# Kernel optimization log

Hardware: AMD Instinct MI355X
Metric: run time of the kernel (lower is better)

The kernel has to match this reference:

```python
import jax, jax.numpy as jnp
import numpy as np

L, D, F, H = 6, 512, 2048, 8
DH = D // H
SCALE = DH ** -0.5
B, S = 2, 2048


def _ln(x, w, b):
    m = jnp.mean(x, axis=-1, keepdims=True)
    v = jnp.var(x, axis=-1, keepdims=True)
    return (x - m) * jax.lax.rsqrt(v + 1e-5) * w + b


def setup_inputs() -> dict:
    key = jax.random.key(0)
    ks = jax.random.split(key, 10)
    s = 0.02
    return {
        "x": jax.random.normal(ks[0], (B, S, D), jnp.float32),
        "mask": jnp.zeros((B, 1, 1, S), jnp.float32),
        "ln1_w": jnp.ones((L, D), jnp.float32),
        "ln1_b": jnp.zeros((L, D), jnp.float32),
        "in_w": s * jax.random.normal(ks[1], (L, D, 3 * D), jnp.float32),
        "in_b": jnp.zeros((L, 3 * D), jnp.float32),
        "out_w": s * jax.random.normal(ks[2], (L, D, D), jnp.float32),
        "out_b": jnp.zeros((L, D), jnp.float32),
        "ln2_w": jnp.ones((L, D), jnp.float32),
        "ln2_b": jnp.zeros((L, D), jnp.float32),
        "ffn1_w": s * jax.random.normal(ks[3], (L, D, F), jnp.float32),
        "ffn1_b": jnp.zeros((L, F), jnp.float32),
        "ffn2_w": s * jax.random.normal(ks[4], (L, F, D), jnp.float32),
        "ffn2_b": jnp.zeros((L, D), jnp.float32),
        "norm_w": jnp.ones((D,), jnp.float32),
        "norm_b": jnp.zeros((D,), jnp.float32),
    }


def reference(x, mask, ln1_w, ln1_b, in_w, in_b, out_w, out_b,
              ln2_w, ln2_b, ffn1_w, ffn1_b, ffn2_w, ffn2_b, norm_w, norm_b):
    def step(h, p):
        (l1w, l1b, iw, ib, ow, ob, l2w, l2b, f1w, f1b, f2w, f2b) = p
        # --- self-attention (pre-norm) ---
        y = _ln(h, l1w, l1b)
        proj = y @ iw + ib                       # [B,S,3D]
        q, k, v = jnp.split(proj, 3, axis=-1)    # each [B,S,D]
        q = q.reshape(B, S, H, DH)
        k = k.reshape(B, S, H, DH)
        v = v.reshape(B, S, H, DH)
        dot = jnp.einsum('bqhd,bkhd->bhqk', q * SCALE, k) + mask  # [B,H,S,S]
        att = jax.nn.softmax(dot, axis=-1)
        o = jnp.einsum('bhqk,bkhd->bqhd', att, v).reshape(B, S, D)
        h = o @ ow + ob + h
        # --- FFN (pre-norm) ---
        y = _ln(h, l2w, l2b)
        y = jax.nn.relu(y @ f1w + f1b) @ f2w + f2b
        return h + y, None

    params = (ln1_w, ln1_b, in_w, in_b, out_w, out_b,
              ln2_w, ln2_b, ffn1_w, ffn1_b, ffn2_w, ffn2_b)
    x, _ = jax.lax.scan(step, x, params)
    return _ln(x, norm_w, norm_b)
```

## Files before the change

kernel.cpp:

```cpp
#include <hip/hip_runtime.h>
#include <hip/hip_bf16.h>
#include <stdint.h>


typedef __bf16 bf16x8 __attribute__((ext_vector_type(8)));
typedef __bf16 bf16x4 __attribute__((ext_vector_type(4)));
typedef float f32x4 __attribute__((ext_vector_type(4)));
typedef unsigned short u16;
typedef unsigned short u16x8 __attribute__((ext_vector_type(8)));

#define NB 2
#define NS 2048
#define ND 512
#define NH 8
#define NDH 64
#define NF 2048
#define NL 6
#define NCHUNK 4
#define CK (NS / NCHUNK)
#define LOG2E 1.4426950408889634f
#define QSCALE (0.125f * LOG2E)

#if defined(__has_builtin)
#if __has_builtin(__builtin_amdgcn_global_load_lds)
#define HAVE_GLDS 1
#endif
#endif
#ifndef HAVE_GLDS
#define HAVE_GLDS 0
#endif

#if HAVE_GLDS
__device__ __forceinline__ void glds16(const u16* g, u16* l) {
  __builtin_amdgcn_global_load_lds(
      (const __attribute__((address_space(1))) unsigned int*)g,
      (__attribute__((address_space(3))) unsigned int*)l, 16, 0, 0);
}
#endif

__device__ __forceinline__ u16 f2bf(float f) {
  unsigned u = __float_as_uint(f);
  u += 0x7FFFu + ((u >> 16) & 1u);
  return (u16)(u >> 16);
}

__device__ __forceinline__ int xswz(int w, int n) {
  return (w & 7) * (n >> 3) + (w >> 3);
}

__global__ __launch_bounds__(256) void wcvt_t(const float* __restrict__ src,
                                              u16* __restrict__ dst,
                                              int K, int N) {
  __shared__ float tile[32][33];
  int l = blockIdx.z;
  const float* s = src + (size_t)l * K * N;
  u16* d = dst + (size_t)l * K * N;
  int k0 = blockIdx.y * 32, n0 = blockIdx.x * 32;
  int tx = threadIdx.x, ty = threadIdx.y;
  for (int i = 0; i < 32; i += 8)
    tile[ty + i][tx] = s[(size_t)(k0 + ty + i) * N + n0 + tx];
  __syncthreads();
  for (int i = 0; i < 32; i += 8)
    d[(size_t)(n0 + ty + i) * K + k0 + tx] = f2bf(tile[tx][ty + i]);
}

template <int OUT_BF16>
__global__ __launch_bounds__(256) void ln_k(const float* __restrict__ x,
                                            const float* __restrict__ w,
                                            const float* __restrict__ b,
                                            void* __restrict__ out) {
  int row = blockIdx.x;
  int t = threadIdx.x;
  const float* xr = x + (size_t)row * ND;
  float2 v = ((const float2*)xr)[t];
  float s = v.x + v.y, ss = v.x * v.x + v.y * v.y;
  for (int o = 32; o > 0; o >>= 1) {
    s += __shfl_down(s, o);
    ss += __shfl_down(ss, o);
  }
  __shared__ float rs[4], rss[4];
  if ((t & 63) == 0) { rs[t >> 6] = s; rss[t >> 6] = ss; }
  __syncthreads();
  float S = rs[0] + rs[1] + rs[2] + rs[3];
  float SS = rss[0] + rss[1] + rss[2] + rss[3];
  float mean = S * (1.0f / ND);
  float var = SS * (1.0f / ND) - mean * mean;
  float rstd = rsqrtf(var + 1e-5f);
  float2 wv = ((const float2*)w)[t];
  float2 bv = ((const float2*)b)[t];
  float y0 = (v.x - mean) * rstd * wv.x + bv.x;
  float y1 = (v.y - mean) * rstd * wv.y + bv.y;
  if (OUT_BF16) {
    ushort2 p; p.x = f2bf(y0); p.y = f2bf(y1);
    ((ushort2*)out)[(size_t)row * (ND / 2) + t] = p;
  } else {
    float2 p; p.x = y0; p.y = y1;
    ((float2*)out)[(size_t)row * (ND / 2) + t] = p;
  }
}

template <int EPI, int BM, int BN, int BK>
__global__ __launch_bounds__(256) void gemm_bt(const u16* __restrict__ A,
                                               const u16* __restrict__ Bt,
                                               const float* __restrict__ bias,
                                               const float* __restrict__ resid,
                                               void* __restrict__ C,
                                               int M, int N, int K) {
  constexpr int MT = BM / 32;
  constexpr int NT = BN / 32;
  constexpr int CB = BK / 8;
  constexpr int RPP = 2048 / BK;
  constexpr int AP = BM / RPP;
  constexpr int BP = BN / RPP;
  constexpr int KK = BK / 32;
  __shared__ u16 la[2][BM * BK];
  __shared__ u16 lb[2][BN * BK];
  int flat = blockIdx.x + gridDim.x * blockIdx.y;
  int s_id = xswz(flat, gridDim.x * gridDim.y);
  int bn = s_id % gridDim.x, bm = s_id / gridDim.x;
  int t = threadIdx.x;
  int wave = t >> 6, lane = t & 63, quad = lane >> 4, l15 = lane & 15;
  int wm = (wave >> 1) * (BM / 2), wn = (wave & 1) * (BN / 2);
  f32x4 acc[MT][NT] = {};
  int srow = t / CB;
  int scol = ((t % CB) ^ (srow & (CB - 1))) * 8;
  const u16* Ag = A + (size_t)(bm * BM) * K;
  const u16* Bg = Bt + (size_t)(bn * BN) * K;

  auto stage = [&](int k0, int buf) {
#if HAVE_GLDS
    u16* laB = &la[buf][0] + wave * 512;
    u16* lbB = &lb[buf][0] + wave * 512;
#pragma unroll
    for (int g = 0; g < AP; g++)
      glds16(&Ag[(size_t)(srow + g * RPP) * K + k0 + scol], laB + g * 2048);
#pragma unroll
    for (int g = 0; g < BP; g++)
      glds16(&Bg[(size_t)(srow + g * RPP) * K + k0 + scol], lbB + g * 2048);
#else
#pragma unroll
    for (int g = 0; g < AP; g++)
      *(bf16x8*)&la[buf][(srow + g * RPP) * BK + (t % CB) * 8] =
          *(const bf16x8*)&Ag[(size_t)(srow + g * RPP) * K + k0 + scol];
#pragma unroll
    for (int g = 0; g < BP; g++)
      *(bf16x8*)&lb[buf][(srow + g * RPP) * BK + (t % CB) * 8] =
          *(const bf16x8*)&Bg[(size_t)(srow + g * RPP) * K + k0 + scol];
#endif
  };

  stage(0, 0);
  const int nk = K / BK;
  int cur = 0;
  for (int ks = 0; ks < nk; ks++) {
    __syncthreads();
    if (ks + 1 < nk) stage((ks + 1) * BK, cur ^ 1);
    const u16* lac = &la[cur][0];
    const u16* lbc = &lb[cur][0];
#pragma unroll
    for (int kk = 0; kk < KK; kk++) {
      bf16x8 af[MT], bfr[NT];
#pragma unroll
      for (int i = 0; i < MT; i++) {
        int row = wm + i * 16 + l15;
        af[i] = *(const bf16x8*)&lac[row * BK + ((kk * 4 + quad) ^ (row & (CB - 1))) * 8];
      }
#pragma unroll
      for (int i = 0; i < NT; i++) {
        int row = wn + i * 16 + l15;
        bfr[i] = *(const bf16x8*)&lbc[row * BK + ((kk * 4 + quad) ^ (row & (CB - 1))) * 8];
      }
#pragma unroll
      for (int mt = 0; mt < MT; mt++)
#pragma unroll
        for (int nt = 0; nt < NT; nt++)
          acc[mt][nt] = __builtin_amdgcn_mfma_f32_16x16x32_bf16(
              af[mt], bfr[nt], acc[mt][nt], 0, 0, 0);
    }
    cur ^= 1;
  }
#pragma unroll
  for (int mt = 0; mt < MT; mt++)
#pragma unroll
    for (int nt = 0; nt < NT; nt++) {
      int col = bn * BN + wn + nt * 16 + l15;
      float bcol = (EPI == 3) ? 0.f : bias[col];
#pragma unroll
      for (int r = 0; r < 4; r++) {
        int row = bm * BM + wm + mt * 16 + quad * 4 + r;
        float v = acc[mt][nt][r] + ((EPI == 3) ? bias[row] : bcol);
        if (EPI == 1) v = fmaxf(v, 0.f);
        if (EPI == 2)
          ((float*)C)[(size_t)row * N + col] = v + resid[(size_t)row * N + col];
        else
          ((u16*)C)[(size_t)row * N + col] = f2bf(v);
      }
    }
}

__global__ __launch_bounds__(256) void attn_k(const u16* __restrict__ qk,
                                              const u16* __restrict__ vt,
                                              const float* __restrict__ mask,
                                              u16* __restrict__ opart,
                                              float* __restrict__ lbuf) {
  __shared__ u16 kt_s[64 * 64];
  __shared__ u16 vt_s[64 * 64];
  __shared__ u16 p_s[4][16 * 64];
  __shared__ float mask_s[CK];
  int flat = blockIdx.x + 32 * (blockIdx.y + 16 * blockIdx.z);
  int s_id = xswz(flat, 32 * 16 * NCHUNK);
  int qt = s_id & 31;
  int bh = (s_id >> 5) & 15;
  int c = s_id >> 9;
  int b = bh >> 3, h = bh & 7;
  int t = threadIdx.x;
  int wave = t >> 6, lane = t & 63, quad = lane >> 4, l15 = lane & 15;

  {
    const float* mrow = mask + b * NS + c * CK;
    mask_s[t] = mrow[t] * LOG2E;
    mask_s[t + 256] = mrow[t + 256] * LOG2E;
  }

  int qrow = qt * 64 + wave * 16 + l15;
  const u16* qbase = qk + ((size_t)(b * NS + qrow)) * (2 * ND) + h * NDH;
  bf16x8 qf[2];
  qf[0] = *(const bf16x8*)&qbase[quad * 8];
  qf[1] = *(const bf16x8*)&qbase[32 + quad * 8];
#pragma unroll
  for (int e = 0; e < 8; e++) {
    qf[0][e] = (__bf16)((float)qf[0][e] * QSCALE);
    qf[1][e] = (__bf16)((float)qf[1][e] * QSCALE);
  }
  bf16x8 ones;
#pragma unroll
  for (int e = 0; e < 8; e++) ones[e] = (__bf16)1.0f;

  f32x4 oacc[4] = {};
  f32x4 ls = {};

  int srow8 = t >> 3;
  int segsw = ((t & 7) ^ ((t >> 3) & 7)) * 8;
  const u16* kg0 = qk + ((size_t)(b * NS + srow8)) * (2 * ND) + ND + h * NDH + segsw;
  const u16* vg0 = vt + ((size_t)(h * NDH + srow8)) * (NB * NS) + b * NS + segsw;
#if HAVE_GLDS
  u16* ktB = kt_s + wave * 512;
  u16* vtB = vt_s + wave * 512;
#endif
  u16* pw = &p_s[wave][0];
  int l7 = l15 & 7;
  for (int kt0 = c * CK; kt0 < (c + 1) * CK; kt0 += 64) {
    __syncthreads();
#if HAVE_GLDS
    glds16(&kg0[(size_t)kt0 * (2 * ND)], ktB);
    glds16(&kg0[(size_t)(kt0 + 32) * (2 * ND)], ktB + 2048);
    glds16(&vg0[kt0], vtB);
    glds16(&vg0[kt0 + (size_t)32 * (NB * NS)], vtB + 2048);
#else
    *(bf16x8*)&kt_s[srow8 * 64 + (t & 7) * 8] =
        *(const bf16x8*)&kg0[(size_t)kt0 * (2 * ND)];
    *(bf16x8*)&kt_s[(srow8 + 32) * 64 + (t & 7) * 8] =
        *(const bf16x8*)&kg0[(size_t)(kt0 + 32) * (2 * ND)];
    *(bf16x8*)&vt_s[srow8 * 64 + (t & 7) * 8] = *(const bf16x8*)&vg0[kt0];
    *(bf16x8*)&vt_s[(srow8 + 32) * 64 + (t & 7) * 8] =
        *(const bf16x8*)&vg0[kt0 + (size_t)32 * (NB * NS)];
#endif
    __syncthreads();
    int ktl = kt0 - c * CK;
    f32x4 sc[4];
#pragma unroll
    for (int nt = 0; nt < 4; nt++)
      sc[nt] = *(const f32x4*)&mask_s[ktl + nt * 16 + quad * 4];
#pragma unroll
    for (int nt = 0; nt < 4; nt++) {
      int row = nt * 16 + l15;
      bf16x8 kf0 = *(const bf16x8*)&kt_s[row * 64 + (quad ^ (row & 7)) * 8];
      bf16x8 kf1 = *(const bf16x8*)&kt_s[row * 64 + ((quad + 4) ^ (row & 7)) * 8];
      sc[nt] = __builtin_amdgcn_mfma_f32_16x16x32_bf16(kf0, qf[0], sc[nt], 0, 0, 0);
      sc[nt] = __builtin_amdgcn_mfma_f32_16x16x32_bf16(kf1, qf[1], sc[nt], 0, 0, 0);
    }
#pragma unroll
    for (int nt = 0; nt < 4; nt++) {
      float2 plo, phi;
      plo.x = __builtin_amdgcn_exp2f(sc[nt][0]);
      plo.y = __builtin_amdgcn_exp2f(sc[nt][1]);
      phi.x = __builtin_amdgcn_exp2f(sc[nt][2]);
      phi.y = __builtin_amdgcn_exp2f(sc[nt][3]);
      __hip_bfloat162 b01 = __float22bfloat162_rn(plo);
      __hip_bfloat162 b23 = __float22bfloat162_rn(phi);
      uint2 pk;
      pk.x = *reinterpret_cast<unsigned int*>(&b01);
      pk.y = *reinterpret_cast<unsigned int*>(&b23);
      int cb = nt * 2 + (quad >> 1);
      int col = ((cb ^ l7) << 3) + (quad & 1) * 4;
      *reinterpret_cast<uint2*>(&pw[l15 * 64 + col]) = pk;
    }
    asm volatile("s_waitcnt lgkmcnt(0)" ::: "memory");
#pragma unroll
    for (int kk = 0; kk < 2; kk++) {
      int cbr = kk * 4 + quad;
      bf16x8 pf = *(const bf16x8*)&pw[l15 * 64 + ((cbr ^ l7) << 3)];
#pragma unroll
      for (int nt = 0; nt < 4; nt++) {
        int row = nt * 16 + l15;
        bf16x8 vf = *(const bf16x8*)&vt_s[row * 64 + ((kk * 4 + quad) ^ (row & 7)) * 8];
        oacc[nt] = __builtin_amdgcn_mfma_f32_16x16x32_bf16(pf, vf, oacc[nt], 0, 0, 0);
      }
      ls = __builtin_amdgcn_mfma_f32_16x16x32_bf16(pf, ones, ls, 0, 0, 0);
    }
  }
  u16* ob = opart + (((size_t)(c * NB * NH + bh) * NS) + qt * 64 + wave * 16) * NDH;
#pragma unroll
  for (int nt = 0; nt < 4; nt++)
#pragma unroll
    for (int r = 0; r < 4; r++)
      ob[(size_t)(quad * 4 + r) * NDH + nt * 16 + l15] = f2bf(oacc[nt][r]);
  if (l15 == 0) {
    size_t li = (size_t)(c * NB * NH + bh) * NS + qt * 64 + wave * 16 + quad * 4;
#pragma unroll
    for (int r = 0; r < 4; r++) lbuf[li + r] = ls[r];
  }
}

__global__ __launch_bounds__(256) void attn_merge(const u16* __restrict__ opart,
                                                  const float* __restrict__ lbuf,
                                                  u16* __restrict__ o) {
  int gt = blockIdx.x * 256 + threadIdx.x;
  int grp = gt & 7;
  int s = (gt >> 3) & (NS - 1);
  int bh = gt >> 14;
  float L = 0.f;
#pragma unroll
  for (int c = 0; c < NCHUNK; c++)
    L += lbuf[(size_t)(c * NB * NH + bh) * NS + s];
  float inv = 1.0f / L;
  float acc[8] = {};
#pragma unroll
  for (int c = 0; c < NCHUNK; c++) {
    bf16x8 ov = *(const bf16x8*)&opart[((size_t)(c * NB * NH + bh) * NS + s) * NDH + grp * 8];
#pragma unroll
    for (int j = 0; j < 8; j++) acc[j] += (float)ov[j];
  }
  u16x8 res;
#pragma unroll
  for (int j = 0; j < 8; j++) res[j] = f2bf(acc[j] * inv);
  int b = bh >> 3, h = bh & 7;
  *(u16x8*)&o[((size_t)(b * NS + s)) * ND + h * NDH + grp * 8] = res;
}

extern "C" void kernel_launch(void* const* d_in, const int* in_sizes, int n_in,
                              void* d_out, int out_size, void* d_ws, size_t ws_size,
                              hipStream_t stream) {
  const float* x = (const float*)d_in[0];
  const float* mask = (const float*)d_in[1];
  const float* ln1w = (const float*)d_in[2];
  const float* ln1b = (const float*)d_in[3];
  const float* in_w = (const float*)d_in[4];
  const float* in_b = (const float*)d_in[5];
  const float* out_w = (const float*)d_in[6];
  const float* out_b = (const float*)d_in[7];
  const float* ln2w = (const float*)d_in[8];
  const float* ln2b = (const float*)d_in[9];
  const float* f1w = (const float*)d_in[10];
  const float* f1b = (const float*)d_in[11];
  const float* f2w = (const float*)d_in[12];
  const float* f2b = (const float*)d_in[13];
  const float* normw = (const float*)d_in[14];
  const float* normb = (const float*)d_in[15];

  char* ws = (char*)d_ws;
  auto carve = [&](size_t bytes) {
    char* p = ws;
    ws += (bytes + 255) & ~(size_t)255;
    return p;
  };
  u16* wq_t = (u16*)carve((size_t)NL * 3 * ND * ND * 2);
  u16* wo_t = (u16*)carve((size_t)NL * ND * ND * 2);
  u16* w1_t = (u16*)carve((size_t)NL * NF * ND * 2);
  u16* w2_t = (u16*)carve((size_t)NL * ND * NF * 2);
  u16* ybuf = (u16*)carve((size_t)NB * NS * ND * 2);
  u16* qk = (u16*)carve((size_t)NB * NS * 2 * ND * 2);
  u16* vtb = (u16*)carve((size_t)ND * NB * NS * 2);
  u16* obuf = (u16*)carve((size_t)NB * NS * ND * 2);
  u16* ubuf = (u16*)carve((size_t)NB * NS * NF * 2);
  float* hA = (float*)carve((size_t)NB * NS * ND * 4);
  float* hB = (float*)carve((size_t)NB * NS * ND * 4);
  float* lbuf = (float*)carve((size_t)NCHUNK * NB * NH * NS * 4);
  u16* opart = ubuf;

  const int M = NB * NS;
  dim3 tb(32, 8);
  wcvt_t<<<dim3(3 * ND / 32, ND / 32, NL), tb, 0, stream>>>(in_w, wq_t, ND, 3 * ND);
  wcvt_t<<<dim3(ND / 32, ND / 32, NL), tb, 0, stream>>>(out_w, wo_t, ND, ND);
  wcvt_t<<<dim3(NF / 32, ND / 32, NL), tb, 0, stream>>>(f1w, w1_t, ND, NF);
  wcvt_t<<<dim3(ND / 32, NF / 32, NL), tb, 0, stream>>>(f2w, w2_t, NF, ND);

  const float* hin = x;
  for (int l = 0; l < NL; l++) {
    ln_k<1><<<M, 256, 0, stream>>>(hin, ln1w + l * ND, ln1b + l * ND, ybuf);
    gemm_bt<0, 64, 128, 64><<<dim3(2 * ND / 128, M / 64), 256, 0, stream>>>(
        ybuf, wq_t + (size_t)l * 3 * ND * ND, in_b + l * 3 * ND, nullptr, qk,
        M, 2 * ND, ND);
    gemm_bt<3, 64, 64, 128><<<dim3(M / 64, ND / 64), 256, 0, stream>>>(
        wq_t + (size_t)l * 3 * ND * ND + (size_t)2 * ND * ND, ybuf,
        in_b + l * 3 * ND + 2 * ND, nullptr, vtb, ND, M, ND);
    attn_k<<<dim3(NS / 64, NB * NH, NCHUNK), 256, 0, stream>>>(
        qk, vtb, mask, opart, lbuf);
    attn_merge<<<(NB * NH * NS * 8) / 256, 256, 0, stream>>>(opart, lbuf, obuf);
    gemm_bt<2, 64, 64, 128><<<dim3(ND / 64, M / 64), 256, 0, stream>>>(
        obuf, wo_t + (size_t)l * ND * ND, out_b + l * ND, hin, hB, M, ND, ND);
    ln_k<1><<<M, 256, 0, stream>>>(hB, ln2w + l * ND, ln2b + l * ND, ybuf);
    gemm_bt<1, 128, 128, 64><<<dim3(NF / 128, M / 128), 256, 0, stream>>>(
        ybuf, w1_t + (size_t)l * NF * ND, f1b + l * NF, nullptr, ubuf, M, NF, ND);
    gemm_bt<2, 64, 64, 128><<<dim3(ND / 64, M / 64), 256, 0, stream>>>(
        ubuf, w2_t + (size_t)l * ND * NF, f2b + l * ND, hB, hA, M, ND, NF);
    hin = hA;
  }
  ln_k<0><<<M, 256, 0, stream>>>(hA, normw, normb, (float*)d_out);
}
```

Before: 763.7 us.

## Split-K the FFN2 GEMM with atomic accumulation into residual-initialised output

The FFN down-projection GEMM (K=2048) is split into two K halves across blockIdx.z, with a smaller 64x64x64 tile, and each half atomically adds its partial result into the fp32 output. The second layernorm kernel now also writes residual plus ffn2 bias into that output buffer, so the atomics only add the matmul contribution. This doubles the block count for a GEMM that previously had only 512 blocks, to fill more CUs, at the cost of fp32 atomic traffic and non-deterministic summation order.

```diff
diff --git a/kernel.cpp b/kernel.cpp
--- a/kernel.cpp
+++ b/kernel.cpp
@@ -64,15 +64,24 @@
     d[(size_t)(n0 + ty + i) * K + k0 + tx] = f2bf(tile[tx][ty + i]);
 }
 
-template <int OUT_BF16>
+template <int MODE>
 __global__ __launch_bounds__(256) void ln_k(const float* __restrict__ x,
                                             const float* __restrict__ w,
                                             const float* __restrict__ b,
-                                            void* __restrict__ out) {
+                                            void* __restrict__ out,
+                                            const float* __restrict__ bias2,
+                                            float* __restrict__ init_out) {
   int row = blockIdx.x;
   int t = threadIdx.x;
   const float* xr = x + (size_t)row * ND;
   float2 v = ((const float2*)xr)[t];
+  if (MODE == 2) {
+    float2 b2 = ((const float2*)bias2)[t];
+    float2 iv;
+    iv.x = v.x + b2.x;
+    iv.y = v.y + b2.y;
+    ((float2*)init_out)[(size_t)row * (ND / 2) + t] = iv;
+  }
   float s = v.x + v.y, ss = v.x * v.x + v.y * v.y;
   for (int o = 32; o > 0; o >>= 1) {
     s += __shfl_down(s, o);
@@ -90,7 +99,7 @@
   float2 bv = ((const float2*)b)[t];
   float y0 = (v.x - mean) * rstd * wv.x + bv.x;
   float y1 = (v.y - mean) * rstd * wv.y + bv.y;
-  if (OUT_BF16) {
+  if (MODE != 0) {
     ushort2 p; p.x = f2bf(y0); p.y = f2bf(y1);
     ((ushort2*)out)[(size_t)row * (ND / 2) + t] = p;
   } else {
@@ -105,7 +114,7 @@
                                                const float* __restrict__ bias,
                                                const float* __restrict__ resid,
                                                void* __restrict__ C,
-                                               int M, int N, int K) {
+                                               int M, int N, int K, int lda) {
   constexpr int MT = BM / 32;
   constexpr int NT = BN / 32;
   constexpr int CB = BK / 8;
@@ -124,8 +133,8 @@
   f32x4 acc[MT][NT] = {};
   int srow = t / CB;
   int scol = ((t % CB) ^ (srow & (CB - 1))) * 8;
-  const u16* Ag = A + (size_t)(bm * BM) * K;
-  const u16* Bg = Bt + (size_t)(bn * BN) * K;
+  const u16* Ag = A + (size_t)(bm * BM) * lda + (size_t)blockIdx.z * K;
+  const u16* Bg = Bt + (size_t)(bn * BN) * lda + (size_t)blockIdx.z * K;
 
   auto stage = [&](int k0, int buf) {
 #if HAVE_GLDS
@@ -133,19 +142,19 @@
     u16* lbB = &lb[buf][0] + wave * 512;
 #pragma unroll
     for (int g = 0; g < AP; g++)
-      glds16(&Ag[(size_t)(srow + g * RPP) * K + k0 + scol], laB + g * 2048);
+      glds16(&Ag[(size_t)(srow + g * RPP) * lda + k0 + scol], laB + g * 2048);
 #pragma unroll
     for (int g = 0; g < BP; g++)
-      glds16(&Bg[(size_t)(srow + g * RPP) * K + k0 + scol], lbB + g * 2048);
+      glds16(&Bg[(size_t)(srow + g * RPP) * lda + k0 + scol], lbB + g * 2048);
 #else
 #pragma unroll
     for (int g = 0; g < AP; g++)
       *(bf16x8*)&la[buf][(srow + g * RPP) * BK + (t % CB) * 8] =
-          *(const bf16x8*)&Ag[(size_t)(srow + g * RPP) * K + k0 + scol];
+          *(const bf16x8*)&Ag[(size_t)(srow + g * RPP) * lda + k0 + scol];
 #pragma unroll
     for (int g = 0; g < BP; g++)
       *(bf16x8*)&lb[buf][(srow + g * RPP) * BK + (t % CB) * 8] =
-          *(const bf16x8*)&Bg[(size_t)(srow + g * RPP) * K + k0 + scol];
+          *(const bf16x8*)&Bg[(size_t)(srow + g * RPP) * lda + k0 + scol];
 #endif
   };
 
@@ -184,7 +193,7 @@
 #pragma unroll
     for (int nt = 0; nt < NT; nt++) {
       int col = bn * BN + wn + nt * 16 + l15;
-      float bcol = (EPI == 3) ? 0.f : bias[col];
+      float bcol = (EPI == 3 || EPI == 4) ? 0.f : bias[col];
 #pragma unroll
       for (int r = 0; r < 4; r++) {
         int row = bm * BM + wm + mt * 16 + quad * 4 + r;
@@ -192,6 +201,8 @@
         if (EPI == 1) v = fmaxf(v, 0.f);
         if (EPI == 2)
           ((float*)C)[(size_t)row * N + col] = v + resid[(size_t)row * N + col];
+        else if (EPI == 4)
+          atomicAdd(&((float*)C)[(size_t)row * N + col], v);
         else
           ((u16*)C)[(size_t)row * N + col] = f2bf(v);
       }
@@ -397,24 +408,28 @@
 
   const float* hin = x;
   for (int l = 0; l < NL; l++) {
-    ln_k<1><<<M, 256, 0, stream>>>(hin, ln1w + l * ND, ln1b + l * ND, ybuf);
+    ln_k<1><<<M, 256, 0, stream>>>(hin, ln1w + l * ND, ln1b + l * ND, ybuf,
+                                   nullptr, nullptr);
     gemm_bt<0, 64, 128, 64><<<dim3(2 * ND / 128, M / 64), 256, 0, stream>>>(
         ybuf, wq_t + (size_t)l * 3 * ND * ND, in_b + l * 3 * ND, nullptr, qk,
-        M, 2 * ND, ND);
+        M, 2 * ND, ND, ND);
     gemm_bt<3, 64, 64, 128><<<dim3(M / 64, ND / 64), 256, 0, stream>>>(
         wq_t + (size_t)l * 3 * ND * ND + (size_t)2 * ND * ND, ybuf,
-        in_b + l * 3 * ND + 2 * ND, nullptr, vtb, ND, M, ND);
+        in_b + l * 3 * ND + 2 * ND, nullptr, vtb, ND, M, ND, ND);
     attn_k<<<dim3(NS / 64, NB * NH, NCHUNK), 256, 0, stream>>>(
         qk, vtb, mask, opart, lbuf);
     attn_merge<<<(NB * NH * NS * 8) / 256, 256, 0, stream>>>(opart, lbuf, obuf);
     gemm_bt<2, 64, 64, 128><<<dim3(ND / 64, M / 64), 256, 0, stream>>>(
-        obuf, wo_t + (size_t)l * ND * ND, out_b + l * ND, hin, hB, M, ND, ND);
-    ln_k<1><<<M, 256, 0, stream>>>(hB, ln2w + l * ND, ln2b + l * ND, ybuf);
+        obuf, wo_t + (size_t)l * ND * ND, out_b + l * ND, hin, hB, M, ND, ND, ND);
+    ln_k<2><<<M, 256, 0, stream>>>(hB, ln2w + l * ND, ln2b + l * ND, ybuf,
+                                   f2b + l * ND, hA);
     gemm_bt<1, 128, 128, 64><<<dim3(NF / 128, M / 128), 256, 0, stream>>>(
-        ybuf, w1_t + (size_t)l * NF * ND, f1b + l * NF, nullptr, ubuf, M, NF, ND);
-    gemm_bt<2, 64, 64, 128><<<dim3(ND / 64, M / 64), 256, 0, stream>>>(
-        ubuf, w2_t + (size_t)l * ND * NF, f2b + l * ND, hB, hA, M, ND, NF);
+        ybuf, w1_t + (size_t)l * NF * ND, f1b + l * NF, nullptr, ubuf,
+        M, NF, ND, ND);
+    gemm_bt<4, 64, 64, 64><<<dim3(ND / 64, M / 64, 2), 256, 0, stream>>>(
+        ubuf, w2_t + (size_t)l * ND * NF, nullptr, nullptr, hA,
+        M, ND, NF / 2, NF);
     hin = hA;
   }
-  ln_k<0><<<M, 256, 0, stream>>>(hA, normw, normb, (float*)d_out);
-}
+  ln_k<0><<<M, 256, 0, stream>>>(hA, normw, normb, (float*)d_out, nullptr, nullptr);
+}
```

After: 826.5 us. 8.2% more time.
